# Kernel optimization log

Measured on AMD Instinct MI355X. Metric: run time of the kernel, lower is better.

The kernel has to match this reference:

```python
import jax, jax.numpy as jnp
import numpy as np

N = 20000       # nodes
E = 320000      # edges (before self-loops)
F_IN = 1024     # num_features
H = 4           # head_num
C = 64          # hidden_size
NC = 4          # n_classes
NEG_SLOPE = 0.2 # PyG GATConv default


def setup_inputs() -> dict:
    key = jax.random.key(0)
    ks = jax.random.split(key, 16)
    def w(k, shape, fan_in):
        return jax.random.normal(k, shape, dtype=jnp.float32) / np.sqrt(fan_in)
    x = jax.random.normal(ks[0], (N, F_IN), dtype=jnp.float32)
    edge_index = jax.random.randint(ks[1], (2, E), 0, N, dtype=jnp.int64)
    return {
        "x": x,
        "edge_index": edge_index,
        # layer 1: F_IN -> H*C, concat
        "w1": w(ks[2], (F_IN, H * C), F_IN),
        "as1": w(ks[3], (H, C), C),
        "ad1": w(ks[4], (H, C), C),
        "b1": jnp.zeros((H * C,), jnp.float32),
        # layer 2: H*C -> H*C, concat
        "w2": w(ks[5], (H * C, H * C), H * C),
        "as2": w(ks[6], (H, C), C),
        "ad2": w(ks[7], (H, C), C),
        "b2": jnp.zeros((H * C,), jnp.float32),
        # out layer: H*C -> C, 1 head, concat=False
        "w3": w(ks[8], (H * C, 1 * C), H * C),
        "as3": w(ks[9], (1, C), C),
        "ad3": w(ks[10], (1, C), C),
        "b3": jnp.zeros((C,), jnp.float32),
        # classifier
        "wc": w(ks[11], (C, NC), C),
        "bc": jnp.zeros((NC,), jnp.float32),
    }


def gat_layer(x, src, dst, W, a_src, a_dst, bias, concat):
    """PyG GATConv (eval mode, self-loops already added to src/dst)."""
    n = x.shape[0]
    Hh, Cc = a_src.shape
    h = (x @ W).reshape(n, Hh, Cc)                       # [N,H,C]
    al_s = jnp.sum(h * a_src[None], axis=-1)             # [N,H]
    al_d = jnp.sum(h * a_dst[None], axis=-1)             # [N,H]
    e = al_s[src] + al_d[dst]                            # [E,H]
    e = jax.nn.leaky_relu(e, NEG_SLOPE)
    # segment softmax over incoming edges of each destination node
    emax = jax.ops.segment_max(e, dst, num_segments=n)   # [N,H]
    ex = jnp.exp(e - emax[dst])
    denom = jax.ops.segment_sum(ex, dst, num_segments=n) # [N,H]
    alpha = ex / (denom[dst] + 1e-16)                    # [E,H]
    msg = h[src] * alpha[..., None]                      # [E,H,C]
    out = jax.ops.segment_sum(msg, dst, num_segments=n)  # [N,H,C]
    if concat:
        out = out.reshape(n, Hh * Cc)
    else:
        out = out.mean(axis=1)
    return out + bias


def reference(x, edge_index, w1, as1, ad1, b1, w2, as2, ad2, b2,
              w3, as3, ad3, b3, wc, bc):
    n = x.shape[0]
    loop = jnp.arange(n, dtype=edge_index.dtype)
    src = jnp.concatenate([edge_index[0], loop])
    dst = jnp.concatenate([edge_index[1], loop])
    out = jax.nn.relu(gat_layer(x, src, dst, w1, as1, ad1, b1, True))
    out = jax.nn.relu(gat_layer(out, src, dst, w2, as2, ad2, b2, True))
    out = gat_layer(out, src, dst, w3, as3, ad3, b3, False)
    return out @ wc + bc                                  # [N, n_classes]
```

## Files before the change

kernel.cpp:

```cpp
#include <hip/hip_runtime.h>

#define N_NODES 20000
#define N_EDGES 320000
#define ET (N_EDGES + N_NODES)
#define F_IN 1024
#define HC 256
#define NC 4

typedef unsigned short ushort_t;
typedef __attribute__((ext_vector_type(8))) short short8;
typedef __attribute__((ext_vector_type(4))) float f32x4;

__device__ inline ushort_t f2bf(float f) {
    unsigned u = __float_as_uint(f);
    unsigned r = (u + 0x7fffu + ((u >> 16) & 1u)) >> 16;
    return (ushort_t)r;
}
__device__ inline float bf2f(ushort_t u) {
    return __uint_as_float(((unsigned)u) << 16);
}

#define GLOAD16(gp, lp) __builtin_amdgcn_global_load_lds( \
    (const __attribute__((address_space(1))) void*)(gp),  \
    (__attribute__((address_space(3))) void*)(lp), 16, 0, 0)

__global__ void count_kernel(const int* __restrict__ ei, int* __restrict__ counts) {
    int e = blockIdx.x * blockDim.x + threadIdx.x;
    if (e >= ET) return;
    int dst = (e < N_EDGES) ? ei[N_EDGES + e] : (e - N_EDGES);
    atomicAdd(&counts[dst], 1);
}

__global__ void scan_kernel(const int* __restrict__ counts, int* __restrict__ row_ptr,
                            int* __restrict__ cursor) {
    __shared__ int sums[1024];
    int t = threadIdx.x;
    const int per = (N_NODES + 1023) / 1024;
    int b = t * per;
    int e = min(b + per, N_NODES);
    int s = 0;
    for (int i = b; i < e; ++i) s += counts[i];
    sums[t] = s;
    __syncthreads();
    for (int off = 1; off < 1024; off <<= 1) {
        int v = (t >= off) ? sums[t - off] : 0;
        __syncthreads();
        sums[t] += v;
        __syncthreads();
    }
    int run = (t == 0) ? 0 : sums[t - 1];
    for (int i = b; i < e; ++i) {
        row_ptr[i] = run;
        cursor[i]  = run;
        run += counts[i];
    }
    if (t == 0) row_ptr[N_NODES] = ET;
}

__global__ void scatter_kernel(const int* __restrict__ ei, int* __restrict__ cursor,
                               int* __restrict__ col) {
    int e = blockIdx.x * blockDim.x + threadIdx.x;
    if (e >= ET) return;
    int src, dst;
    if (e < N_EDGES) { src = ei[e]; dst = ei[N_EDGES + e]; }
    else             { src = dst = e - N_EDGES; }
    int pos = atomicAdd(&cursor[dst], 1);
    col[pos] = src;
}

__global__ void split_rows(const float* __restrict__ in, ushort_t* __restrict__ hi,
                           ushort_t* __restrict__ lo, int n4) {
    int i = blockIdx.x * blockDim.x + threadIdx.x;
    int stride = gridDim.x * blockDim.x;
    for (; i < n4; i += stride) {
        float4 v = ((const float4*)in)[i];
        ushort4 h, l;
        h.x = f2bf(v.x); l.x = f2bf(v.x - bf2f(h.x));
        h.y = f2bf(v.y); l.y = f2bf(v.y - bf2f(h.y));
        h.z = f2bf(v.z); l.z = f2bf(v.z - bf2f(h.z));
        h.w = f2bf(v.w); l.w = f2bf(v.w - bf2f(h.w));
        ((ushort4*)hi)[i] = h;
        ((ushort4*)lo)[i] = l;
    }
}

__global__ void split_T(const float* __restrict__ in, ushort_t* __restrict__ hi,
                        ushort_t* __restrict__ lo, int K, int Nn) {
    int idx = blockIdx.x * blockDim.x + threadIdx.x;
    if (idx >= K * Nn) return;
    int k = idx / Nn, n = idx - k * Nn;
    float v = in[idx];
    ushort_t h = f2bf(v);
    hi[(size_t)n * K + k] = h;
    lo[(size_t)n * K + k] = f2bf(v - bf2f(h));
}

template<int BM, int BN, int GY>
__launch_bounds__(256)
__global__ void gemm_mfma(const ushort_t* __restrict__ Ah, const ushort_t* __restrict__ Al,
                          const ushort_t* __restrict__ BTh, const ushort_t* __restrict__ BTl,
                          float* __restrict__ C, int M, int K, int NT) {
    constexpr int SM = BM / 2;
    constexpr int SN = BN / 2;
    constexpr int MF = SM / 16;
    constexpr int NF = SN / 16;
    constexpr int AQ = BM / 64;
    constexpr int BQ = BN / 64;
    __shared__ __align__(16) ushort_t smem[(2 * BM + 2 * BN) * 32];
    char* Ash = (char*)smem;
    char* Asl = Ash + BM * 64;
    char* Bsh = Asl + BM * 64;
    char* Bsl = Bsh + BN * 64;

    const int t = threadIdx.x, lane = t & 63, w = t >> 6;
    const int wm = w >> 1, wn = w & 1;
    const int nwg = gridDim.x;
    const int id = blockIdx.x;
    const int q = nwg >> 3, r = nwg & 7;
    const int xcd = id & 7, idx = id >> 3;
    const int logical = (xcd < r ? xcd * (q + 1) : r * (q + 1) + (xcd - r) * q) + idx;
    const int bm = (logical / GY) * BM, bn = (logical % GY) * BN;
    const int gchunk = ((lane & 3) ^ ((lane >> 3) & 3)) * 16;

    size_t gA[AQ]; int lA[AQ];
    #pragma unroll
    for (int qq = 0; qq < AQ; ++qq) {
        int inst = w * AQ + qq;
        int row  = inst * 16 + (lane >> 2);
        int grow = min(bm + row, M - 1);
        gA[qq] = (size_t)grow * K * 2 + gchunk;
        lA[qq] = inst * 1024;
    }
    size_t gB[BQ]; int lB[BQ];
    #pragma unroll
    for (int qq = 0; qq < BQ; ++qq) {
        int inst = w * BQ + qq;
        int row  = inst * 16 + (lane >> 2);
        gB[qq] = (size_t)(bn + row) * K * 2 + gchunk;
        lB[qq] = inst * 1024;
    }

    f32x4 acc[MF][NF];
    #pragma unroll
    for (int i = 0; i < MF; ++i)
        #pragma unroll
        for (int j = 0; j < NF; ++j) acc[i][j] = (f32x4){0.f, 0.f, 0.f, 0.f};

    const char* Ahb = (const char*)Ah;
    const char* Alb = (const char*)Al;
    const char* Bhb = (const char*)BTh;
    const char* Blb = (const char*)BTl;
    const int c16 = (lane >> 4);

    for (int k0 = 0; k0 < K; k0 += 32) {
        size_t kb = (size_t)k0 * 2;
        #pragma unroll
        for (int qq = 0; qq < AQ; ++qq) {
            GLOAD16(Ahb + gA[qq] + kb, Ash + lA[qq]);
            GLOAD16(Alb + gA[qq] + kb, Asl + lA[qq]);
        }
        #pragma unroll
        for (int qq = 0; qq < BQ; ++qq) {
            GLOAD16(Bhb + gB[qq] + kb, Bsh + lB[qq]);
            GLOAD16(Blb + gB[qq] + kb, Bsl + lB[qq]);
        }
        __syncthreads();
        short8 afh[MF], afl[MF], bfh[NF], bfl[NF];
        #pragma unroll
        for (int i = 0; i < MF; ++i) {
            int row = wm * SM + i * 16 + (lane & 15);
            int off = row * 64 + ((c16 ^ ((row >> 1) & 3)) * 16);
            afh[i] = *(const short8*)(Ash + off);
            afl[i] = *(const short8*)(Asl + off);
        }
        #pragma unroll
        for (int j = 0; j < NF; ++j) {
            int row = wn * SN + j * 16 + (lane & 15);
            int off = row * 64 + ((c16 ^ ((row >> 1) & 3)) * 16);
            bfh[j] = *(const short8*)(Bsh + off);
            bfl[j] = *(const short8*)(Bsl + off);
        }
        #pragma unroll
        for (int i = 0; i < MF; ++i)
            #pragma unroll
            for (int j = 0; j < NF; ++j) {
                acc[i][j] = __builtin_amdgcn_mfma_f32_16x16x32_bf16(afh[i], bfh[j], acc[i][j], 0, 0, 0);
                acc[i][j] = __builtin_amdgcn_mfma_f32_16x16x32_bf16(afh[i], bfl[j], acc[i][j], 0, 0, 0);
                acc[i][j] = __builtin_amdgcn_mfma_f32_16x16x32_bf16(afl[i], bfh[j], acc[i][j], 0, 0, 0);
            }
        __syncthreads();
    }
    #pragma unroll
    for (int i = 0; i < MF; ++i) {
        int rbase = bm + wm * SM + i * 16 + (lane >> 4) * 4;
        #pragma unroll
        for (int j = 0; j < NF; ++j) {
            int col = bn + wn * SN + j * 16 + (lane & 15);
            #pragma unroll
            for (int rr = 0; rr < 4; ++rr)
                if (rbase + rr < M) C[(size_t)(rbase + rr) * NT + col] = acc[i][j][rr];
        }
    }
}

template<int H>
__global__ void al_kernel(const float* __restrict__ h, const float* __restrict__ as_w,
                          const float* __restrict__ ad_w, float* __restrict__ als,
                          float* __restrict__ ald) {
    int n = blockIdx.x;
    int t = threadIdx.x;
    float hv = h[(size_t)n * (H * 64) + t];
    float s = hv * as_w[t];
    float d = hv * ad_w[t];
    #pragma unroll
    for (int off = 32; off > 0; off >>= 1) {
        s += __shfl_down(s, off, 64);
        d += __shfl_down(d, off, 64);
    }
    if ((t & 63) == 0) {
        int head = t >> 6;
        als[n * H + head] = s;
        ald[n * H + head] = d;
    }
}

template<int H>
__launch_bounds__(256)
__global__ void alpha_kernel(const float* __restrict__ als, const float* __restrict__ ald,
                             const int* __restrict__ row_ptr, const int* __restrict__ col,
                             float* __restrict__ alpha) {
    int lane = threadIdx.x & 63, w = threadIdx.x >> 6;
    int dst = blockIdx.x * 4 + w;
    if (dst >= N_NODES) return;
    int beg = row_ptr[dst], deg = row_ptr[dst + 1] - beg;
    constexpr int ES = 64 / H;
    int i_loc = lane / H, hh = lane % H;
    float ad = ald[dst * H + hh];
    float m = -1e30f, den = 0.f;
    for (int base = 0; base < deg; base += ES) {
        int i = base + i_loc;
        if (i < deg) {
            float e = als[col[beg + i] * H + hh] + ad;
            e = (e > 0.f) ? e : 0.2f * e;
            float nm = fmaxf(m, e);
            den = den * __expf(m - nm) + __expf(e - nm);
            m = nm;
        }
    }
    #pragma unroll
    for (int off = H; off < 64; off <<= 1) {
        float mo = __shfl_xor(m, off, 64);
        float dn = __shfl_xor(den, off, 64);
        float nm = fmaxf(m, mo);
        den = den * __expf(m - nm) + dn * __expf(mo - nm);
        m = nm;
    }
    float rden = 1.f / (den + 1e-16f);
    for (int base = 0; base < deg; base += ES) {
        int i = base + i_loc;
        if (i < deg) {
            float e = als[col[beg + i] * H + hh] + ad;
            e = (e > 0.f) ? e : 0.2f * e;
            alpha[(size_t)hh * ET + beg + i] = __expf(e - m) * rden;
        }
    }
}

template<int CT, int CW, int H, bool RELU, bool SPLIT>
__launch_bounds__(256)
__global__ void agg_v3(const float* __restrict__ h, const float* __restrict__ alpha,
                       const int* __restrict__ row_ptr, const int* __restrict__ col,
                       const float* __restrict__ bias,
                       ushort_t* __restrict__ oh, ushort_t* __restrict__ ol,
                       float* __restrict__ of) {
    constexpr int NS  = CT / CW;
    constexpr int LPT = CW / 4;
    constexpr int TPW = 64 / LPT;
    static_assert(NS == H, "slice==head mapping");
    __shared__ int   s_src[4][64];
    __shared__ float s_alp[4][64];
    const int nwg = gridDim.x;
    const int q = nwg >> 3;
    int id = blockIdx.x;
    int logical = (id & 7) * q + (id >> 3);
    int slice = logical / (N_NODES / 4);
    int g = logical - slice * (N_NODES / 4);
    int lane = threadIdx.x & 63, w = threadIdx.x >> 6;
    int dst = g * 4 + w;
    int beg = row_ptr[dst], deg = row_ptr[dst + 1] - beg;
    int team = lane / LPT;
    int cc = (lane & (LPT - 1)) * 4;

    const int*   colP = col + beg;
    const float* aP   = alpha + (size_t)slice * ET + beg;
    const float* hS   = h + slice * CW + cc;

    float4 acc = make_float4(0.f, 0.f, 0.f, 0.f);
    for (int base = 0; base < deg; base += 64) {
        int cnt = min(64, deg - base);
        if (lane < cnt) {
            s_src[w][lane] = colP[base + lane];
            s_alp[w][lane] = aP[base + lane];
        }
        for (int i = team; i < cnt; i += TPW) {
            int   s = s_src[w][i];
            float a = s_alp[w][i];
            float4 hv = *(const float4*)&hS[s * CT];
            acc.x += a * hv.x; acc.y += a * hv.y;
            acc.z += a * hv.z; acc.w += a * hv.w;
        }
    }
    #pragma unroll
    for (int off = LPT; off < 64; off <<= 1) {
        acc.x += __shfl_xor(acc.x, off, 64);
        acc.y += __shfl_xor(acc.y, off, 64);
        acc.z += __shfl_xor(acc.z, off, 64);
        acc.w += __shfl_xor(acc.w, off, 64);
    }
    if (team == 0) {
        int ch = slice * CW + cc;
        float4 bv = *(const float4*)&bias[ch];
        float v0 = acc.x + bv.x, v1 = acc.y + bv.y, v2 = acc.z + bv.z, v3 = acc.w + bv.w;
        if (RELU) {
            v0 = fmaxf(v0, 0.f); v1 = fmaxf(v1, 0.f);
            v2 = fmaxf(v2, 0.f); v3 = fmaxf(v3, 0.f);
        }
        size_t idx = (size_t)dst * CT + ch;
        if (SPLIT) {
            ushort4 h4, l4;
            h4.x = f2bf(v0); l4.x = f2bf(v0 - bf2f(h4.x));
            h4.y = f2bf(v1); l4.y = f2bf(v1 - bf2f(h4.y));
            h4.z = f2bf(v2); l4.z = f2bf(v2 - bf2f(h4.z));
            h4.w = f2bf(v3); l4.w = f2bf(v3 - bf2f(h4.w));
            *(ushort4*)&oh[idx] = h4;
            *(ushort4*)&ol[idx] = l4;
        } else {
            *(float4*)&of[idx] = make_float4(v0, v1, v2, v3);
        }
    }
}

__global__ void classifier_kernel(const float* __restrict__ x, const float* __restrict__ wc,
                                  const float* __restrict__ bc, float* __restrict__ out) {
    int n = blockIdx.x * blockDim.x + threadIdx.x;
    if (n >= N_NODES) return;
    float acc[NC] = {bc[0], bc[1], bc[2], bc[3]};
    for (int c = 0; c < 64; ++c) {
        float xv = x[(size_t)n * 64 + c];
        #pragma unroll
        for (int k = 0; k < NC; ++k) acc[k] += xv * wc[c * NC + k];
    }
    #pragma unroll
    for (int k = 0; k < NC; ++k) out[(size_t)n * NC + k] = acc[k];
}

extern "C" void kernel_launch(void* const* d_in, const int* in_sizes, int n_in,
                              void* d_out, int out_size, void* d_ws, size_t ws_size,
                              hipStream_t stream) {
    const float* x   = (const float*)d_in[0];
    const int*   ei  = (const int*)d_in[1];
    const float* w1  = (const float*)d_in[2];
    const float* as1 = (const float*)d_in[3];
    const float* ad1 = (const float*)d_in[4];
    const float* b1  = (const float*)d_in[5];
    const float* w2  = (const float*)d_in[6];
    const float* as2 = (const float*)d_in[7];
    const float* ad2 = (const float*)d_in[8];
    const float* b2  = (const float*)d_in[9];
    const float* w3  = (const float*)d_in[10];
    const float* as3 = (const float*)d_in[11];
    const float* ad3 = (const float*)d_in[12];
    const float* b3  = (const float*)d_in[13];
    const float* wc  = (const float*)d_in[14];
    const float* bc  = (const float*)d_in[15];
    float* out = (float*)d_out;

    char* ws = (char*)d_ws;
    size_t off = 0;
    auto alloc = [&](size_t bytes) -> char* {
        char* p = ws + off;
        off = (off + bytes + 255) & ~(size_t)255;
        return p;
    };

    int* counts  = (int*)alloc(N_NODES * 4);
    int* cursor  = (int*)alloc(N_NODES * 4);
    int* row_ptr = (int*)alloc((N_NODES + 1) * 4);
    int* colidx  = (int*)alloc(ET * 4);
    float* als   = (float*)alloc(N_NODES * 4 * 4);
    float* ald   = (float*)alloc(N_NODES * 4 * 4);
    float* alpha = (float*)alloc((size_t)4 * ET * 4);
    float* B0    = (float*)alloc((size_t)N_NODES * HC * 4);

    ushort_t* xh   = (ushort_t*)alloc((size_t)N_NODES * F_IN * 2);
    ushort_t* xl   = (ushort_t*)alloc((size_t)N_NODES * F_IN * 2);
    ushort_t* w1Th = (ushort_t*)alloc((size_t)F_IN * HC * 2);
    ushort_t* w1Tl = (ushort_t*)alloc((size_t)F_IN * HC * 2);
    ushort_t* w2Th = (ushort_t*)alloc((size_t)HC * HC * 2);
    ushort_t* w2Tl = (ushort_t*)alloc((size_t)HC * HC * 2);
    ushort_t* w3Th = (ushort_t*)alloc((size_t)HC * 64 * 2);
    ushort_t* w3Tl = (ushort_t*)alloc((size_t)HC * 64 * 2);
    ushort_t* B1h  = (ushort_t*)alloc((size_t)N_NODES * HC * 2);
    ushort_t* B1l  = (ushort_t*)alloc((size_t)N_NODES * HC * 2);
    float*    B1f  = (float*)alloc((size_t)N_NODES * 64 * 4);

    hipMemsetAsync(counts, 0, N_NODES * sizeof(int), stream);
    int eb = (ET + 255) / 256;
    count_kernel<<<eb, 256, 0, stream>>>(ei, counts);
    scan_kernel<<<1, 1024, 0, stream>>>(counts, row_ptr, cursor);
    scatter_kernel<<<eb, 256, 0, stream>>>(ei, cursor, colidx);

    split_rows<<<2048, 256, 0, stream>>>(x, xh, xl, (int)((size_t)N_NODES * F_IN / 4));
    split_T<<<(F_IN * HC + 255) / 256, 256, 0, stream>>>(w1, w1Th, w1Tl, F_IN, HC);
    split_T<<<(HC * HC + 255) / 256, 256, 0, stream>>>(w2, w2Th, w2Tl, HC, HC);
    split_T<<<(HC * 64 + 255) / 256, 256, 0, stream>>>(w3, w3Th, w3Tl, HC, 64);

    const int nwg12 = ((N_NODES + 127) / 128) * (HC / 64);
    const int nblk_dst = N_NODES / 4;
    gemm_mfma<128, 64, 4><<<nwg12, 256, 0, stream>>>(xh, xl, w1Th, w1Tl, B0, N_NODES, F_IN, HC);
    al_kernel<4><<<N_NODES, 256, 0, stream>>>(B0, as1, ad1, als, ald);
    alpha_kernel<4><<<nblk_dst, 256, 0, stream>>>(als, ald, row_ptr, colidx, alpha);
    agg_v3<256, 64, 4, true, true><<<4 * nblk_dst, 256, 0, stream>>>(
        B0, alpha, row_ptr, colidx, b1, B1h, B1l, nullptr);
    gemm_mfma<128, 64, 4><<<nwg12, 256, 0, stream>>>(B1h, B1l, w2Th, w2Tl, B0, N_NODES, HC, HC);
    al_kernel<4><<<N_NODES, 256, 0, stream>>>(B0, as2, ad2, als, ald);
    alpha_kernel<4><<<nblk_dst, 256, 0, stream>>>(als, ald, row_ptr, colidx, alpha);
    agg_v3<256, 64, 4, true, true><<<4 * nblk_dst, 256, 0, stream>>>(
        B0, alpha, row_ptr, colidx, b2, B1h, B1l, nullptr);
    const int nwg3 = (N_NODES + 63) / 64;
    gemm_mfma<64, 64, 1><<<nwg3, 256, 0, stream>>>(B1h, B1l, w3Th, w3Tl, B0, N_NODES, HC, 64);
    al_kernel<1><<<N_NODES, 64, 0, stream>>>(B0, as3, ad3, als, ald);
    alpha_kernel<1><<<nblk_dst, 256, 0, stream>>>(als, ald, row_ptr, colidx, alpha);
    agg_v3<64, 64, 1, false, false><<<nblk_dst, 256, 0, stream>>>(
        B0, alpha, row_ptr, colidx, b3, nullptr, nullptr, B1f);
    classifier_kernel<<<(N_NODES + 255) / 256, 256, 0, stream>>>(B1f, wc, bc, out);
}
```

Baseline: 334.8 us.

## Fuse x bf16 hi/lo split into first GEMM and shrink tile to 64x64

Drops the separate split_rows pass over the 20000x1024 fp32 input, which wrote bf16 hi/lo copies that the first GEMM then read back. A new GEMM kernel loads fp32 x directly, splits it into hi/lo in registers and stores the halves to LDS. The layer-2 GEMM also moves to 64x64 tiles for more workgroups. The tradeoff is that the A operand now uses synchronous register loads plus conversion inside the K loop with no async prefetch, which may expose more latency per iteration.

```diff
diff --git a/kernel.cpp b/kernel.cpp
--- a/kernel.cpp
+++ b/kernel.cpp
@@ -68,22 +68,6 @@
     col[pos] = src;
 }
 
-__global__ void split_rows(const float* __restrict__ in, ushort_t* __restrict__ hi,
-                           ushort_t* __restrict__ lo, int n4) {
-    int i = blockIdx.x * blockDim.x + threadIdx.x;
-    int stride = gridDim.x * blockDim.x;
-    for (; i < n4; i += stride) {
-        float4 v = ((const float4*)in)[i];
-        ushort4 h, l;
-        h.x = f2bf(v.x); l.x = f2bf(v.x - bf2f(h.x));
-        h.y = f2bf(v.y); l.y = f2bf(v.y - bf2f(h.y));
-        h.z = f2bf(v.z); l.z = f2bf(v.z - bf2f(h.z));
-        h.w = f2bf(v.w); l.w = f2bf(v.w - bf2f(h.w));
-        ((ushort4*)hi)[i] = h;
-        ((ushort4*)lo)[i] = l;
-    }
-}
-
 __global__ void split_T(const float* __restrict__ in, ushort_t* __restrict__ hi,
                         ushort_t* __restrict__ lo, int K, int Nn) {
     int idx = blockIdx.x * blockDim.x + threadIdx.x;
@@ -93,6 +77,102 @@
     ushort_t h = f2bf(v);
     hi[(size_t)n * K + k] = h;
     lo[(size_t)n * K + k] = f2bf(v - bf2f(h));
+}
+
+template<int GY>
+__launch_bounds__(256)
+__global__ void gemm_f32a(const float* __restrict__ X,
+                          const ushort_t* __restrict__ BTh, const ushort_t* __restrict__ BTl,
+                          float* __restrict__ C, int M, int K, int NT) {
+    constexpr int BM = 64, BN = 64, SM = 32, SN = 32, MF = 2, NF = 2;
+    __shared__ __align__(16) ushort_t smem[4 * 64 * 32];
+    char* Ash = (char*)smem;
+    char* Asl = Ash + 64 * 64;
+    char* Bsh = Asl + 64 * 64;
+    char* Bsl = Bsh + 64 * 64;
+
+    const int t = threadIdx.x, lane = t & 63, w = t >> 6;
+    const int wm = w >> 1, wn = w & 1;
+    const int nwg = gridDim.x;
+    const int id = blockIdx.x;
+    const int q = nwg >> 3, r = nwg & 7;
+    const int xcd = id & 7, idx = id >> 3;
+    const int logical = (xcd < r ? xcd * (q + 1) : r * (q + 1) + (xcd - r) * q) + idx;
+    const int bm = (logical / GY) * BM, bn = (logical % GY) * BN;
+
+    const int arow = w * 16 + (lane >> 2);
+    const int achk = lane & 3;
+    const int grow = min(bm + arow, M - 1);
+    const float* xRow = X + (size_t)grow * K + achk * 8;
+    const int aoff = arow * 64 + ((achk ^ ((arow >> 1) & 3)) * 16);
+
+    const int gchunk = ((lane & 3) ^ ((lane >> 3) & 3)) * 16;
+    const int brow = w * 16 + (lane >> 2);
+    size_t gB = (size_t)(bn + brow) * K * 2 + gchunk;
+    int lB = w * 1024;
+
+    f32x4 acc[MF][NF];
+    #pragma unroll
+    for (int i = 0; i < MF; ++i)
+        #pragma unroll
+        for (int j = 0; j < NF; ++j) acc[i][j] = (f32x4){0.f, 0.f, 0.f, 0.f};
+
+    const char* Bhb = (const char*)BTh;
+    const char* Blb = (const char*)BTl;
+    const int c16 = (lane >> 4);
+
+    for (int k0 = 0; k0 < K; k0 += 32) {
+        float4 v0 = *(const float4*)(xRow + k0);
+        float4 v1 = *(const float4*)(xRow + k0 + 4);
+        ushort_t hh[8], ll[8];
+        float vv[8] = {v0.x, v0.y, v0.z, v0.w, v1.x, v1.y, v1.z, v1.w};
+        #pragma unroll
+        for (int u = 0; u < 8; ++u) {
+            hh[u] = f2bf(vv[u]);
+            ll[u] = f2bf(vv[u] - bf2f(hh[u]));
+        }
+        *(short8*)(Ash + aoff) = *(short8*)hh;
+        *(short8*)(Asl + aoff) = *(short8*)ll;
+        size_t kb = (size_t)k0 * 2;
+        GLOAD16(Bhb + gB + kb, Bsh + lB);
+        GLOAD16(Blb + gB + kb, Bsl + lB);
+        __syncthreads();
+        short8 afh[MF], afl[MF], bfh[NF], bfl[NF];
+        #pragma unroll
+        for (int i = 0; i < MF; ++i) {
+            int row = wm * SM + i * 16 + (lane & 15);
+            int off = row * 64 + ((c16 ^ ((row >> 1) & 3)) * 16);
+            afh[i] = *(const short8*)(Ash + off);
+            afl[i] = *(const short8*)(Asl + off);
+        }
+        #pragma unroll
+        for (int j = 0; j < NF; ++j) {
+            int row = wn * SN + j * 16 + (lane & 15);
+            int off = row * 64 + ((c16 ^ ((row >> 1) & 3)) * 16);
+            bfh[j] = *(const short8*)(Bsh + off);
+            bfl[j] = *(const short8*)(Bsl + off);
+        }
+        #pragma unroll
+        for (int i = 0; i < MF; ++i)
+            #pragma unroll
+            for (int j = 0; j < NF; ++j) {
+                acc[i][j] = __builtin_amdgcn_mfma_f32_16x16x32_bf16(afh[i], bfh[j], acc[i][j], 0, 0, 0);
+                acc[i][j] = __builtin_amdgcn_mfma_f32_16x16x32_bf16(afh[i], bfl[j], acc[i][j], 0, 0, 0);
+                acc[i][j] = __builtin_amdgcn_mfma_f32_16x16x32_bf16(afl[i], bfh[j], acc[i][j], 0, 0, 0);
+            }
+        __syncthreads();
+    }
+    #pragma unroll
+    for (int i = 0; i < MF; ++i) {
+        int rbase = bm + wm * SM + i * 16 + (lane >> 4) * 4;
+        #pragma unroll
+        for (int j = 0; j < NF; ++j) {
+            int col = bn + wn * SN + j * 16 + (lane & 15);
+            #pragma unroll
+            for (int rr = 0; rr < 4; ++rr)
+                if (rbase + rr < M) C[(size_t)(rbase + rr) * NT + col] = acc[i][j][rr];
+        }
+    }
 }
 
 template<int BM, int BN, int GY>
@@ -392,8 +472,6 @@
     float* alpha = (float*)alloc((size_t)4 * ET * 4);
     float* B0    = (float*)alloc((size_t)N_NODES * HC * 4);
 
-    ushort_t* xh   = (ushort_t*)alloc((size_t)N_NODES * F_IN * 2);
-    ushort_t* xl   = (ushort_t*)alloc((size_t)N_NODES * F_IN * 2);
     ushort_t* w1Th = (ushort_t*)alloc((size_t)F_IN * HC * 2);
     ushort_t* w1Tl = (ushort_t*)alloc((size_t)F_IN * HC * 2);
     ushort_t* w2Th = (ushort_t*)alloc((size_t)HC * HC * 2);
@@ -410,19 +488,18 @@
     scan_kernel<<<1, 1024, 0, stream>>>(counts, row_ptr, cursor);
     scatter_kernel<<<eb, 256, 0, stream>>>(ei, cursor, colidx);
 
-    split_rows<<<2048, 256, 0, stream>>>(x, xh, xl, (int)((size_t)N_NODES * F_IN / 4));
     split_T<<<(F_IN * HC + 255) / 256, 256, 0, stream>>>(w1, w1Th, w1Tl, F_IN, HC);
     split_T<<<(HC * HC + 255) / 256, 256, 0, stream>>>(w2, w2Th, w2Tl, HC, HC);
     split_T<<<(HC * 64 + 255) / 256, 256, 0, stream>>>(w3, w3Th, w3Tl, HC, 64);
 
-    const int nwg12 = ((N_NODES + 127) / 128) * (HC / 64);
+    const int nwg64 = ((N_NODES + 63) / 64) * (HC / 64);
     const int nblk_dst = N_NODES / 4;
-    gemm_mfma<128, 64, 4><<<nwg12, 256, 0, stream>>>(xh, xl, w1Th, w1Tl, B0, N_NODES, F_IN, HC);
+    gemm_f32a<4><<<nwg64, 256, 0, stream>>>(x, w1Th, w1Tl, B0, N_NODES, F_IN, HC);
     al_kernel<4><<<N_NODES, 256, 0, stream>>>(B0, as1, ad1, als, ald);
     alpha_kernel<4><<<nblk_dst, 256, 0, stream>>>(als, ald, row_ptr, colidx, alpha);
     agg_v3<256, 64, 4, true, true><<<4 * nblk_dst, 256, 0, stream>>>(
         B0, alpha, row_ptr, colidx, b1, B1h, B1l, nullptr);
-    gemm_mfma<128, 64, 4><<<nwg12, 256, 0, stream>>>(B1h, B1l, w2Th, w2Tl, B0, N_NODES, HC, HC);
+    gemm_mfma<64, 64, 4><<<nwg64, 256, 0, stream>>>(B1h, B1l, w2Th, w2Tl, B0, N_NODES, HC, HC);
     al_kernel<4><<<N_NODES, 256, 0, stream>>>(B0, as2, ad2, als, ald);
     alpha_kernel<4><<<nblk_dst, 256, 0, stream>>>(als, ald, row_ptr, colidx, alpha);
     agg_v3<256, 64, 4, true, true><<<4 * nblk_dst, 256, 0, stream>>>(
```

Result: faster. 316.9 us (-5.3%).
